# Performance work log

Measured on AMD Instinct MI355X. Metric: run time of the kernel, lower is better.

Reference implementation:

```python
import jax, jax.numpy as jnp
import numpy as np

NUM_EXPERTS = 8
TOP_K = 2


def setup_inputs() -> dict:
    key = jax.random.key(0)
    ks = jax.random.split(key, 6)
    B, S, D, H, E = 4, 1024, 1024, 2048, NUM_EXPERTS
    x = jax.random.normal(ks[0], (B, S, D), dtype=jnp.float32)
    Wg = jax.random.normal(ks[1], (D, E), dtype=jnp.float32) * 0.02
    W1 = jax.random.normal(ks[2], (E, D, H), dtype=jnp.float32) * 0.02
    b1 = jax.random.normal(ks[3], (E, H), dtype=jnp.float32) * 0.02
    W2 = jax.random.normal(ks[4], (E, H, D), dtype=jnp.float32) * 0.02
    b2 = jax.random.normal(ks[5], (E, D), dtype=jnp.float32) * 0.02
    return {"x": x, "Wg": Wg, "W1": W1, "b1": b1, "W2": W2, "b2": b2}


def reference(x, Wg, W1, b1, W2, b2):
    B, S, D = x.shape
    E, _, H = W1.shape
    OUT = W2.shape[2]
    xm = x.reshape(-1, D)                      # [N, D], N = B*S
    # --- top-k gating (ProbabilitySamplerTopk): softmax over experts, take top-k ---
    logits = xm @ Wg                           # [N, E]
    probs = jax.nn.softmax(logits, axis=-1)
    topk_p, topk_i = jax.lax.top_k(probs, TOP_K)   # [N, K]
    # --- sort dispatched (token, expert) pairs by expert id (stable) ---
    flat_e = topk_i.reshape(-1)                # [N*K]
    flat_p = topk_p.reshape(-1)                # [N*K]
    order = jnp.argsort(flat_e)                # stable sort -> grouped by expert
    tok_idx = order // TOP_K                   # source token index (trunc-div by topK)
    e_sorted = flat_e[order]                   # [N*K]
    p_sorted = flat_p[order]                   # [N*K]
    xs = xm[tok_idx]                           # [N*K, D] expert-sorted inputs
    # --- grouped-GEMM experts: masked per-expert dense GEMM (E is small & fixed) ---
    y = jnp.zeros((xs.shape[0], OUT), dtype=xs.dtype)
    for e in range(E):
        h = jax.nn.relu(xs @ W1[e] + b1[e])    # [N*K, H]
        ye = h @ W2[e] + b2[e]                 # [N*K, OUT]
        m = (e_sorted == e)[:, None].astype(xs.dtype)
        y = y + m * ye
    # --- combine: multiply by gates, scatter-add back to token slots ---
    y = y * p_sorted[:, None]
    out = jnp.zeros((B * S, OUT), dtype=y.dtype).at[tok_idx].add(y)
    return out.reshape(B, S, OUT)
```

## Files before the change

kernel.cpp:

```cpp
#include <hip/hip_runtime.h>
#include <hip/hip_bf16.h>
#include <stdint.h>

typedef __bf16 bf16;
typedef __bf16 bf16x8 __attribute__((ext_vector_type(8)));
typedef __bf16 bf16x4 __attribute__((ext_vector_type(4)));
typedef float f32x4 __attribute__((ext_vector_type(4)));

#define N_TOK 4096
#define DDIM 1024
#define HDIM 2048
#define NPAIR 8192

__device__ __forceinline__ void gload16(const void* g, void* l) {
  __builtin_amdgcn_global_load_lds(
      (const __attribute__((address_space(1))) unsigned int*)g,
      (__attribute__((address_space(3))) unsigned int*)l, 16, 0, 0);
}

__global__ void transpose_cvt_kernel(const float* __restrict__ in, bf16* __restrict__ out,
                                     int R, int C) {
  __shared__ float tile[32][33];
  const float* ip = in + (size_t)blockIdx.z * R * C;
  bf16* op = out + (size_t)blockIdx.z * R * C;
  int r0 = blockIdx.y * 32, c0 = blockIdx.x * 32;
  int tr = threadIdx.x >> 3;
  int tc = (threadIdx.x & 7) * 4;
  float4 v = *(const float4*)(ip + (size_t)(r0 + tr) * C + c0 + tc);
  tile[tr][tc] = v.x; tile[tr][tc + 1] = v.y; tile[tr][tc + 2] = v.z; tile[tr][tc + 3] = v.w;
  __syncthreads();
  bf16x4 o = {(bf16)tile[tc + 0][tr], (bf16)tile[tc + 1][tr],
              (bf16)tile[tc + 2][tr], (bf16)tile[tc + 3][tr]};
  *(bf16x4*)(op + (size_t)(c0 + tr) * R + r0 + tc) = o;
}

__global__ void gate_kernel(const float* __restrict__ x, const float* __restrict__ Wg,
                            int2* __restrict__ ge, float2* __restrict__ gp,
                            bf16* __restrict__ xb, float* __restrict__ outp) {
  int t0 = blockIdx.x * 4;
  {
    float4 z = make_float4(0.f, 0.f, 0.f, 0.f);
    float4* ob = (float4*)(outp + (size_t)t0 * DDIM);
#pragma unroll
    for (int r = 0; r < 4; r++) ob[r * 256 + threadIdx.x] = z;
  }
  int t = t0 + (threadIdx.x >> 6);
  int lane = threadIdx.x & 63;
  const float* xr = x + (size_t)t * DDIM;
  bf16* xbr = xb + (size_t)t * DDIM;
  float a[8];
#pragma unroll
  for (int e = 0; e < 8; e++) a[e] = 0.f;
#pragma unroll
  for (int it = 0; it < 4; it++) {
    int d0 = it * 256 + lane * 4;
    float4 xv = *(const float4*)(xr + d0);
    bf16x4 o = {(bf16)xv.x, (bf16)xv.y, (bf16)xv.z, (bf16)xv.w};
    *(bf16x4*)(xbr + d0) = o;
    float xs[4] = {xv.x, xv.y, xv.z, xv.w};
#pragma unroll
    for (int dd = 0; dd < 4; dd++) {
      float4 w0 = *(const float4*)(Wg + (size_t)(d0 + dd) * 8);
      float4 w1 = *(const float4*)(Wg + (size_t)(d0 + dd) * 8 + 4);
      a[0] += xs[dd] * w0.x; a[1] += xs[dd] * w0.y; a[2] += xs[dd] * w0.z; a[3] += xs[dd] * w0.w;
      a[4] += xs[dd] * w1.x; a[5] += xs[dd] * w1.y; a[6] += xs[dd] * w1.z; a[7] += xs[dd] * w1.w;
    }
  }
#pragma unroll
  for (int off = 32; off >= 1; off >>= 1) {
#pragma unroll
    for (int e = 0; e < 8; e++) a[e] += __shfl_xor(a[e], off);
  }
  if (lane == 0) {
    float m = a[0];
#pragma unroll
    for (int e = 1; e < 8; e++) m = fmaxf(m, a[e]);
    float p[8]; float s = 0.f;
#pragma unroll
    for (int e = 0; e < 8; e++) { p[e] = expf(a[e] - m); s += p[e]; }
    float inv = 1.f / s;
    int i0 = 0; float v0 = a[0];
#pragma unroll
    for (int e = 1; e < 8; e++) if (a[e] > v0) { v0 = a[e]; i0 = e; }
    int i1 = -1; float v1 = -1e30f;
#pragma unroll
    for (int e = 0; e < 8; e++) if (e != i0 && a[e] > v1) { v1 = a[e]; i1 = e; }
    ge[t] = make_int2(i0, i1);
    gp[t] = make_float2(p[i0] * inv, p[i1] * inv);
  }
}

__global__ void sort_kernel(const int2* __restrict__ ge, const float2* __restrict__ gp,
                            int* __restrict__ tok, float* __restrict__ ps,
                            int* __restrict__ meta) {
  __shared__ int hist[8], runn[8], wc[16][8], wb[16][8], baseS[9];
  int tid = threadIdx.x;
  int lane = tid & 63, wv = tid >> 6;
  if (tid < 8) hist[tid] = 0;
  __syncthreads();
  for (int i = tid; i < NPAIR; i += 1024) {
    int2 g = ge[i >> 1];
    int e = (i & 1) ? g.y : g.x;
    atomicAdd(&hist[e], 1);
  }
  __syncthreads();
  if (tid == 0) {
    int b = 0, ts1 = 0;
    for (int e = 0; e < 8; e++) {
      baseS[e] = b; meta[e] = b;
      meta[9 + e] = ts1;  ts1 += (hist[e] + 127) / 128;
      b += hist[e];
    }
    baseS[8] = b; meta[8] = b; meta[17] = ts1;
  }
  __syncthreads();
  if (tid < 8) runn[tid] = baseS[tid];
  __syncthreads();
  for (int c = 0; c < 8; c++) {
    int i = c * 1024 + tid;
    int2 g = ge[i >> 1];
    int e = (i & 1) ? g.y : g.x;
    int rank = 0;
#pragma unroll
    for (int ee = 0; ee < 8; ee++) {
      unsigned long long b = __ballot(e == ee);
      if (e == ee) rank = __popcll(b & ((1ull << lane) - 1ull));
      if (lane == 0) wc[wv][ee] = __popcll(b);
    }
    __syncthreads();
    if (tid < 8) {
      int s = runn[tid];
      for (int w = 0; w < 16; w++) { wb[w][tid] = s; s += wc[w][tid]; }
      runn[tid] = s;
    }
    __syncthreads();
    int pos = wb[wv][e] + rank;
    tok[pos] = i >> 1;
    float2 p2 = gp[i >> 1];
    ps[pos] = (i & 1) ? p2.y : p2.x;
    __syncthreads();
  }
}

template <int KDIM, int NPE, bool FIRST, int NT>
__global__ __launch_bounds__(256, 3)
void moe_gemm_kernel(const bf16* __restrict__ A, const bf16* __restrict__ Bt,
                     const float* __restrict__ bias, const int* __restrict__ tok,
                     const float* __restrict__ ps, const int* __restrict__ meta,
                     bf16* __restrict__ hout, float* __restrict__ outp) {
  __shared__ bf16 lds[3][8192];

  int MTa = meta[17];
  int xcd = blockIdx.x & 7;
  int idx = blockIdx.x >> 3;
  int mLo = (MTa * xcd) >> 3;
  int mHi = (MTa * (xcd + 1)) >> 3;
  int cnt = mHi - mLo;
  if (idx >= cnt * NT) return;
  int tileN = idx / cnt;
  int tileM = mLo + idx - tileN * cnt;

  int e = 0;
#pragma unroll
  for (int k = 1; k < 8; k++) if (tileM >= meta[9 + k]) e = k;
  int row0 = meta[e] + (tileM - meta[9 + e]) * 128;
  int segEnd = meta[e + 1];
  int n0 = tileN * 128;

  int t = threadIdx.x;
  const bf16* aSrc[2];
  const bf16* bSrc[2];
  {
    int swz = ((t & 3) ^ ((t >> 3) & 3)) * 8;
#pragma unroll
    for (int r = 0; r < 2; r++) {
      int row = r * 64 + (t >> 2);
      int gRow = row0 + row; if (gRow > NPAIR - 1) gRow = NPAIR - 1;
      int arow = FIRST ? tok[gRow] : gRow;
      aSrc[r] = A + (size_t)arow * KDIM + swz;
      bSrc[r] = Bt + ((size_t)e * NPE + n0 + row) * KDIM + swz;
    }
  }

  int lane = t & 63, wv = t >> 6;
  int wm = wv >> 1, wn = wv & 1;
  int l15 = lane & 15, l4 = lane >> 4;
  int aOff[4], bOff[4];
#pragma unroll
  for (int m = 0; m < 4; m++) {
    int row = wm * 64 + m * 16 + l15;
    aOff[m] = row * 32 + ((l4 ^ ((row >> 1) & 3)) * 8);
  }
#pragma unroll
  for (int n = 0; n < 4; n++) {
    int row = wn * 64 + n * 16 + l15;
    bOff[n] = 4096 + row * 32 + ((l4 ^ ((row >> 1) & 3)) * 8);
  }

  f32x4 acc[4][4];
#pragma unroll
  for (int m = 0; m < 4; m++)
#pragma unroll
    for (int n = 0; n < 4; n++)
#pragma unroll
      for (int j = 0; j < 4; j++) acc[m][n][j] = 0.f;

  auto STAGE = [&](int kt, int slot) {
    bf16* sb = &lds[slot][0];
    int ko = kt * 32;
    gload16(aSrc[0] + ko, sb + t * 8);
    gload16(aSrc[1] + ko, sb + 2048 + t * 8);
    gload16(bSrc[0] + ko, sb + 4096 + t * 8);
    gload16(bSrc[1] + ko, sb + 6144 + t * 8);
  };

  constexpr int nk = KDIM / 32;
  STAGE(0, 0);
  STAGE(1, 1);
  for (int kt = 0; kt < nk; kt++) {
    if (kt == nk - 1) asm volatile("s_waitcnt vmcnt(0)\n\ts_barrier" ::: "memory");
    else              asm volatile("s_waitcnt vmcnt(4)\n\ts_barrier" ::: "memory");
    if (kt + 2 < nk) STAGE(kt + 2, (kt + 2) % 3);
    __builtin_amdgcn_sched_barrier(0);
    const bf16* sb = &lds[kt % 3][0];
    bf16x8 af[4], bfr[4];
#pragma unroll
    for (int m = 0; m < 4; m++) af[m] = *(const bf16x8*)(sb + aOff[m]);
#pragma unroll
    for (int n = 0; n < 4; n++) bfr[n] = *(const bf16x8*)(sb + bOff[n]);
    __builtin_amdgcn_s_setprio(1);
#pragma unroll
    for (int m = 0; m < 4; m++)
#pragma unroll
      for (int n = 0; n < 4; n++)
        acc[m][n] = __builtin_amdgcn_mfma_f32_16x16x32_bf16(af[m], bfr[n], acc[m][n], 0, 0, 0);
    __builtin_amdgcn_s_setprio(0);
  }

  int colb = n0 + wn * 64 + l15;
  int rowb = wm * 64 + l4 * 4;
  float bia[4];
#pragma unroll
  for (int n = 0; n < 4; n++) bia[n] = bias[(size_t)e * NPE + colb + n * 16];
#pragma unroll
  for (int m = 0; m < 4; m++) {
#pragma unroll
    for (int j = 0; j < 4; j++) {
      int gRow = row0 + rowb + m * 16 + j;
      if (gRow < segEnd) {
        if (FIRST) {
#pragma unroll
          for (int n = 0; n < 4; n++) {
            float v = acc[m][n][j] + bia[n];
            v = fmaxf(v, 0.f);
            hout[(size_t)gRow * NPE + colb + n * 16] = (bf16)v;
          }
        } else {
          float pscale = ps[gRow];
          float* orow = outp + (size_t)tok[gRow] * DDIM;
#pragma unroll
          for (int n = 0; n < 4; n++) {
            float v = (acc[m][n][j] + bia[n]) * pscale;
            atomicAdd(orow + colb + n * 16, v);
          }
        }
      }
    }
  }
}

extern "C" void kernel_launch(void* const* d_in, const int* in_sizes, int n_in,
                              void* d_out, int out_size, void* d_ws, size_t ws_size,
                              hipStream_t stream) {
  (void)in_sizes; (void)n_in; (void)out_size; (void)ws_size;
  const float* x  = (const float*)d_in[0];
  const float* Wg = (const float*)d_in[1];
  const float* W1 = (const float*)d_in[2];
  const float* b1 = (const float*)d_in[3];
  const float* W2 = (const float*)d_in[4];
  const float* b2 = (const float*)d_in[5];
  float* out = (float*)d_out;

  char* ws = (char*)d_ws;
  bf16*  xb   = (bf16*)(ws);
  bf16*  W1T  = (bf16*)(ws + (8ull  << 20));
  bf16*  W2T  = (bf16*)(ws + (40ull << 20));
  bf16*  hbuf = (bf16*)(ws + (72ull << 20));
  char*  ext  = ws + (104ull << 20);
  int2*   ge      = (int2*)(ext);
  float2* gp      = (float2*)(ext + (64u  << 10));
  int*    tok     = (int*)(ext + (128u << 10));
  float*  psarr   = (float*)(ext + (160u << 10));
  int*    meta    = (int*)(ext + (224u << 10));

  transpose_cvt_kernel<<<dim3(64, 32, 8), 256, 0, stream>>>(W1, W1T, 1024, 2048);
  transpose_cvt_kernel<<<dim3(32, 64, 8), 256, 0, stream>>>(W2, W2T, 2048, 1024);
  gate_kernel<<<1024, 256, 0, stream>>>(x, Wg, ge, gp, xb, out);
  sort_kernel<<<1, 1024, 0, stream>>>(ge, gp, tok, psarr, meta);
  moe_gemm_kernel<1024, 2048, true, 16><<<dim3(1152), 256, 0, stream>>>(
      xb, W1T, b1, tok, psarr, meta, hbuf, nullptr);
  moe_gemm_kernel<2048, 1024, false, 8><<<dim3(576), 256, 0, stream>>>(
      hbuf, W2T, b2, tok, psarr, meta, nullptr, out);
}
```

Measured before the change: 197.8 us.

## Widen MoE GEMM tiles to 128x256 with split-phase load/MFMA interleave

Raises the GEMM block tile from 128x128 to 128x256, so each wave accumulates a 64x128 sub-tile and the A tile is reused across twice as many output columns. The grid is halved accordingly and occupancy drops to two blocks per CU to fit the larger LDS buffers and accumulators. The k-loop is split into two MFMA half-phases, with the B-tile global loads spread between them to overlap memory traffic with compute. The larger tile risks fewer blocks than CUs (288 for the second GEMM), higher register pressure and extra barriers per k-step.

```diff
diff --git a/kernel.cpp b/kernel.cpp
--- a/kernel.cpp
+++ b/kernel.cpp
@@ -143,12 +143,13 @@
 }
 
 template <int KDIM, int NPE, bool FIRST, int NT>
-__global__ __launch_bounds__(256, 3)
+__global__ __launch_bounds__(256, 2)
 void moe_gemm_kernel(const bf16* __restrict__ A, const bf16* __restrict__ Bt,
                      const float* __restrict__ bias, const int* __restrict__ tok,
                      const float* __restrict__ ps, const int* __restrict__ meta,
                      bf16* __restrict__ hout, float* __restrict__ outp) {
-  __shared__ bf16 lds[3][8192];
+  __shared__ bf16 lds[3][12288];
+  constexpr int nk = KDIM / 32;
 
   int MTa = meta[17];
   int xcd = blockIdx.x & 7;
@@ -165,69 +166,74 @@
   for (int k = 1; k < 8; k++) if (tileM >= meta[9 + k]) e = k;
   int row0 = meta[e] + (tileM - meta[9 + e]) * 128;
   int segEnd = meta[e + 1];
-  int n0 = tileN * 128;
+  int n0 = tileN * 256;
 
   int t = threadIdx.x;
+  int swz = ((t & 3) ^ ((t >> 3) & 3)) * 8;
   const bf16* aSrc[2];
-  const bf16* bSrc[2];
-  {
-    int swz = ((t & 3) ^ ((t >> 3) & 3)) * 8;
-#pragma unroll
-    for (int r = 0; r < 2; r++) {
-      int row = r * 64 + (t >> 2);
-      int gRow = row0 + row; if (gRow > NPAIR - 1) gRow = NPAIR - 1;
-      int arow = FIRST ? tok[gRow] : gRow;
-      aSrc[r] = A + (size_t)arow * KDIM + swz;
-      bSrc[r] = Bt + ((size_t)e * NPE + n0 + row) * KDIM + swz;
-    }
+  const bf16* bSrc[4];
+#pragma unroll
+  for (int u = 0; u < 2; u++) {
+    int row = u * 64 + (t >> 2);
+    int gRow = row0 + row; if (gRow > NPAIR - 1) gRow = NPAIR - 1;
+    int arow = FIRST ? tok[gRow] : gRow;
+    aSrc[u] = A + (size_t)arow * KDIM + swz;
+  }
+#pragma unroll
+  for (int u = 0; u < 4; u++) {
+    int row = u * 64 + (t >> 2);
+    bSrc[u] = Bt + ((size_t)e * NPE + n0 + row) * KDIM + swz;
   }
 
   int lane = t & 63, wv = t >> 6;
   int wm = wv >> 1, wn = wv & 1;
   int l15 = lane & 15, l4 = lane >> 4;
-  int aOff[4], bOff[4];
+  int aOff[4], bOff[8];
 #pragma unroll
   for (int m = 0; m < 4; m++) {
     int row = wm * 64 + m * 16 + l15;
     aOff[m] = row * 32 + ((l4 ^ ((row >> 1) & 3)) * 8);
   }
 #pragma unroll
-  for (int n = 0; n < 4; n++) {
-    int row = wn * 64 + n * 16 + l15;
+  for (int n = 0; n < 8; n++) {
+    int row = wn * 128 + n * 16 + l15;
     bOff[n] = 4096 + row * 32 + ((l4 ^ ((row >> 1) & 3)) * 8);
   }
 
-  f32x4 acc[4][4];
+  f32x4 acc[4][8];
 #pragma unroll
   for (int m = 0; m < 4; m++)
 #pragma unroll
-    for (int n = 0; n < 4; n++)
+    for (int n = 0; n < 8; n++)
 #pragma unroll
       for (int j = 0; j < 4; j++) acc[m][n][j] = 0.f;
 
-  auto STAGE = [&](int kt, int slot) {
-    bf16* sb = &lds[slot][0];
-    int ko = kt * 32;
-    gload16(aSrc[0] + ko, sb + t * 8);
-    gload16(aSrc[1] + ko, sb + 2048 + t * 8);
-    gload16(bSrc[0] + ko, sb + 4096 + t * 8);
-    gload16(bSrc[1] + ko, sb + 6144 + t * 8);
+  auto SA = [&](int j, int u) {
+    gload16(aSrc[u] + j * 32, &lds[j % 3][0] + u * 2048 + t * 8);
   };
-
-  constexpr int nk = KDIM / 32;
-  STAGE(0, 0);
-  STAGE(1, 1);
-  for (int kt = 0; kt < nk; kt++) {
-    if (kt == nk - 1) asm volatile("s_waitcnt vmcnt(0)\n\ts_barrier" ::: "memory");
-    else              asm volatile("s_waitcnt vmcnt(4)\n\ts_barrier" ::: "memory");
-    if (kt + 2 < nk) STAGE(kt + 2, (kt + 2) % 3);
+  auto SB = [&](int j, int u) {
+    gload16(bSrc[u] + j * 32, &lds[j % 3][0] + 4096 + u * 2048 + t * 8);
+  };
+
+  SA(0, 0); SA(0, 1); SB(0, 0); SB(0, 1); SB(0, 2); SB(0, 3);
+  SA(1, 0); SA(1, 1); SB(1, 0); SB(1, 1); SB(1, 2); SB(1, 3);
+  asm volatile("s_waitcnt vmcnt(6)\n\ts_barrier" ::: "memory");
+
+  for (int j = 0; j < nk; j++) {
+    const bf16* sb = &lds[j % 3][0];
+    bf16x8 af[4], bfr[4];
+#pragma unroll
+    for (int m = 0; m < 4; m++) af[m] = *(const bf16x8*)(sb + aOff[m]);
+#pragma unroll
+    for (int n = 0; n < 4; n++) bfr[n] = *(const bf16x8*)(sb + bOff[n]);
+    if (j + 2 < nk) {
+      SA(j + 2, 0); SA(j + 2, 1); SB(j + 2, 0);
+      asm volatile("s_waitcnt vmcnt(3)\n\ts_barrier" ::: "memory");
+    } else {
+      asm volatile("s_waitcnt vmcnt(0)\n\ts_barrier" ::: "memory");
+    }
+    asm volatile("s_waitcnt lgkmcnt(0)" ::: "memory");
     __builtin_amdgcn_sched_barrier(0);
-    const bf16* sb = &lds[kt % 3][0];
-    bf16x8 af[4], bfr[4];
-#pragma unroll
-    for (int m = 0; m < 4; m++) af[m] = *(const bf16x8*)(sb + aOff[m]);
-#pragma unroll
-    for (int n = 0; n < 4; n++) bfr[n] = *(const bf16x8*)(sb + bOff[n]);
     __builtin_amdgcn_s_setprio(1);
 #pragma unroll
     for (int m = 0; m < 4; m++)
@@ -235,23 +241,37 @@
       for (int n = 0; n < 4; n++)
         acc[m][n] = __builtin_amdgcn_mfma_f32_16x16x32_bf16(af[m], bfr[n], acc[m][n], 0, 0, 0);
     __builtin_amdgcn_s_setprio(0);
-  }
-
-  int colb = n0 + wn * 64 + l15;
-  int rowb = wm * 64 + l4 * 4;
-  float bia[4];
-#pragma unroll
-  for (int n = 0; n < 4; n++) bia[n] = bias[(size_t)e * NPE + colb + n * 16];
+    __builtin_amdgcn_s_barrier();
+#pragma unroll
+    for (int n = 0; n < 4; n++) bfr[n] = *(const bf16x8*)(sb + bOff[4 + n]);
+    if (j + 2 < nk) { SB(j + 2, 1); SB(j + 2, 2); SB(j + 2, 3); }
+    __builtin_amdgcn_s_barrier();
+    asm volatile("s_waitcnt lgkmcnt(0)" ::: "memory");
+    __builtin_amdgcn_sched_barrier(0);
+    __builtin_amdgcn_s_setprio(1);
+#pragma unroll
+    for (int m = 0; m < 4; m++)
+#pragma unroll
+      for (int n = 0; n < 4; n++)
+        acc[m][4 + n] = __builtin_amdgcn_mfma_f32_16x16x32_bf16(af[m], bfr[n], acc[m][4 + n], 0, 0, 0);
+    __builtin_amdgcn_s_setprio(0);
+    __builtin_amdgcn_s_barrier();
+  }
+
+  int colb = n0 + wn * 128 + l15;
+  float bia[8];
+#pragma unroll
+  for (int n = 0; n < 8; n++) bia[n] = bias[(size_t)e * NPE + colb + n * 16];
 #pragma unroll
   for (int m = 0; m < 4; m++) {
 #pragma unroll
-    for (int j = 0; j < 4; j++) {
-      int gRow = row0 + rowb + m * 16 + j;
+    for (int jj = 0; jj < 4; jj++) {
+      int gRow = row0 + wm * 64 + m * 16 + l4 * 4 + jj;
       if (gRow < segEnd) {
         if (FIRST) {
 #pragma unroll
-          for (int n = 0; n < 4; n++) {
-            float v = acc[m][n][j] + bia[n];
+          for (int n = 0; n < 8; n++) {
+            float v = acc[m][n][jj] + bia[n];
             v = fmaxf(v, 0.f);
             hout[(size_t)gRow * NPE + colb + n * 16] = (bf16)v;
           }
@@ -259,8 +279,8 @@
           float pscale = ps[gRow];
           float* orow = outp + (size_t)tok[gRow] * DDIM;
 #pragma unroll
-          for (int n = 0; n < 4; n++) {
-            float v = (acc[m][n][j] + bia[n]) * pscale;
+          for (int n = 0; n < 8; n++) {
+            float v = (acc[m][n][jj] + bia[n]) * pscale;
             atomicAdd(orow + colb + n * 16, v);
           }
         }
@@ -297,8 +317,8 @@
   transpose_cvt_kernel<<<dim3(32, 64, 8), 256, 0, stream>>>(W2, W2T, 2048, 1024);
   gate_kernel<<<1024, 256, 0, stream>>>(x, Wg, ge, gp, xb, out);
   sort_kernel<<<1, 1024, 0, stream>>>(ge, gp, tok, psarr, meta);
-  moe_gemm_kernel<1024, 2048, true, 16><<<dim3(1152), 256, 0, stream>>>(
+  moe_gemm_kernel<1024, 2048, true, 8><<<dim3(576), 256, 0, stream>>>(
       xb, W1T, b1, tok, psarr, meta, hbuf, nullptr);
-  moe_gemm_kernel<2048, 1024, false, 8><<<dim3(576), 256, 0, stream>>>(
+  moe_gemm_kernel<2048, 1024, false, 4><<<dim3(288), 256, 0, stream>>>(
       hbuf, W2T, b2, tok, psarr, meta, nullptr, out);
 }
```

Result: slower. 203.1 us (+2.7%).
